# Optimization experiments

Hardware: AMD Instinct MI355X
Metric: run time of the kernel (lower is better)

Reference implementation:

```python
import jax, jax.numpy as jnp
import numpy as np

DIM = 1024
NUM_HEADS = 8
HEAD_DIM = 64
QK_DIM = NUM_HEADS * HEAD_DIM  # 512
B, S = 4, 1024


def setup_inputs() -> dict:
    key = jax.random.key(0)
    k1, k2, k3, k4, k5 = jax.random.split(key, 5)
    x = jax.random.normal(k1, (B, S, DIM), dtype=jnp.float32)
    mask = jax.random.randint(k2, (B, S), 0, 2).astype(bool)
    rotator = jax.random.normal(k3, (B, S, HEAD_DIM, HEAD_DIM), dtype=jnp.float32)
    # Linear weights stored as [in, out] for x @ W
    w_t = jax.random.normal(k4, (DIM, 2 * QK_DIM + DIM), dtype=jnp.float32) * (DIM ** -0.5)
    w_o = jax.random.normal(k5, (DIM, DIM), dtype=jnp.float32) * (DIM ** -0.5)
    return {"x": x, "mask": mask, "rotator": rotator, "w_t": w_t, "w_o": w_o}


def taylor_atn_fn(qs, ks, vs, mask):
    # 2nd-order Taylor approximation of softmax attention:
    # exp(s) ~= 1 + s + s^2/2, with invalid keys masked out.
    scale = HEAD_DIM ** -0.5
    s = jnp.einsum('bqhd,bkhd->bhqk', qs, ks) * scale  # [B,H,S,S]
    scores = 1.0 + s + 0.5 * s * s
    scores = scores * mask[:, None, None, :].astype(scores.dtype)  # mask keys
    denom = jnp.maximum(jnp.sum(scores, axis=-1), 1e-6)            # [B,H,Q]
    out = jnp.einsum('bhqk,bkhd->bqhd', scores, vs)
    out = out / jnp.transpose(denom, (0, 2, 1))[..., None]         # [B,Q,H,vd]
    return out.reshape(out.shape[0], out.shape[1], -1)


def reference(x, mask, rotator, w_t, w_o):
    t = x @ w_t                                   # [B,S,2*QK+DIM]
    Bx, Sx = t.shape[0], t.shape[1]
    qs = t[..., :QK_DIM].reshape(Bx, Sx, NUM_HEADS, HEAD_DIM)
    ks = t[..., QK_DIM:2 * QK_DIM].reshape(Bx, Sx, NUM_HEADS, HEAD_DIM)
    vs = t[..., 2 * QK_DIM:].reshape(Bx, Sx, NUM_HEADS, -1)
    m = mask[..., None, None]
    # masked per-position rotation: q -> R q, k -> R^T k
    qs = jnp.where(m, jnp.einsum('bsij,bshj->bshi', rotator, qs), qs)
    ks = jnp.where(m, jnp.einsum('bsij,bshi->bshj', rotator, ks), ks)
    out = taylor_atn_fn(qs, ks, vs, mask)
    return out @ w_o
```

## Files before the change

kernel.cpp:

```cpp
#include <hip/hip_runtime.h>
#include <cstdint>
#include <cstddef>

#define DIMX  1024
#define NH    8
#define HD    64
#define QKD   512
#define VDD   128
#define BATCH 4
#define SEQ   1024
#define NPOS  (BATCH*SEQ)
#define TW    (2*QKD + DIMX)
#define SCALE 0.125f

typedef __bf16 bf16x8 __attribute__((ext_vector_type(8)));
typedef float  f32x4  __attribute__((ext_vector_type(4)));
typedef float  f32x16 __attribute__((ext_vector_type(16)));

__device__ __forceinline__ ushort f2bf(float f) {
    unsigned b = __float_as_uint(f);
    return (ushort)((b + 0x7FFFu + ((b >> 16) & 1u)) >> 16);
}
__device__ __forceinline__ float bf2f(ushort u) {
    return __uint_as_float((unsigned)u << 16);
}

__device__ __forceinline__ unsigned cvtpk(float lo, float hi) {
    unsigned r;
    asm("v_cvt_pk_bf16_f32 %0, %1, %2" : "=v"(r) : "v"(lo), "v"(hi));
    return r;
}

__device__ __forceinline__ void plswap(unsigned &a, unsigned &b) {
    asm("v_permlane32_swap_b32 %0, %1" : "+v"(a), "+v"(b));
}

#define GLD16(src, dst) __builtin_amdgcn_global_load_lds(                      \
    (const __attribute__((address_space(1))) unsigned int*)(src),              \
    (__attribute__((address_space(3))) unsigned int*)(dst), 16, 0, 0)

#define SW(row, col) ((row)*64 + ((col) ^ (((row)&7)<<3)))

__device__ __forceinline__ int2 xcd_swz(int gx, int gy) {
    const int nwg = gx * gy;
    int id = blockIdx.y * gx + blockIdx.x;
    id = (id & 7) * (nwg >> 3) + (id >> 3);
    return make_int2(id % gx, id / gx);
}

__global__ __launch_bounds__(256)
void prep_all(const float* __restrict__ x, const float* __restrict__ w_t,
              const float* __restrict__ w_o, const int* __restrict__ mask,
              ushort* __restrict__ xbf, ushort* __restrict__ wtT,
              ushort* __restrict__ woT, int* __restrict__ cpos,
              int* __restrict__ nvalid)
{
    __shared__ float tile[32][33];
    const int bid = blockIdx.x;
    if (bid >= 5120) {
        const int b = bid - 5120;
        int* part = (int*)tile;
        const int t = threadIdx.x;
        int4 m = *(const int4*)(mask + b*SEQ + t*4);
        const int v0 = (m.x != 0), v1 = (m.y != 0);
        const int v2 = (m.z != 0), v3 = (m.w != 0);
        const int mine = v0 + v1 + v2 + v3;
        part[t] = mine;
        __syncthreads();
        for (int off = 1; off < 256; off <<= 1) {
            int y = (t >= off) ? part[t - off] : 0;
            __syncthreads();
            part[t] += y;
            __syncthreads();
        }
        const int ex = part[t] - mine;
        int4 o;
        o.x = v0 ? ex : -1;
        o.y = v1 ? ex + v0 : -1;
        o.z = v2 ? ex + v0 + v1 : -1;
        o.w = v3 ? ex + v0 + v1 + v2 : -1;
        *(int4*)(cpos + b*SEQ + t*4) = o;
        if (t == 255) nvalid[b] = part[255];
        return;
    }
    if (bid < 2048) {
        const size_t i = ((size_t)bid * 256 + threadIdx.x) * 8;
        float4 v0 = *(const float4*)(x + i);
        float4 v1 = *(const float4*)(x + i + 4);
        ushort o[8] = {f2bf(v0.x), f2bf(v0.y), f2bf(v0.z), f2bf(v0.w),
                       f2bf(v1.x), f2bf(v1.y), f2bf(v1.z), f2bf(v1.w)};
        *(uint4*)(xbf + i) = *(uint4*)o;
        return;
    }
    const float* W; ushort* WT; int K, N, bn, bk;
    if (bid < 4096) {
        W = w_t; WT = wtT; K = DIMX; N = TW;
        const int t = bid - 2048;
        bn = (t & 63) * 32; bk = (t >> 6) * 32;
    } else {
        W = w_o; WT = woT; K = DIMX; N = DIMX;
        const int t = bid - 4096;
        bn = (t & 31) * 32; bk = (t >> 5) * 32;
    }
    const int tx = threadIdx.x & 31;
    const int ty = threadIdx.x >> 5;
    #pragma unroll
    for (int i = ty; i < 32; i += 8)
        tile[i][tx] = W[(size_t)(bk + i) * N + bn + tx];
    __syncthreads();
    #pragma unroll
    for (int i = ty; i < 32; i += 8)
        WT[(size_t)(bn + i) * K + bk + tx] = f2bf(tile[tx][i]);
}

#define GEMM_PROLOGUE(Aptr, Bptr, Kdim)                                        \
    __shared__ __align__(16) ushort lA[2 * 128 * 64];                          \
    __shared__ __align__(16) ushort lB[2 * 128 * 64];                          \
    const int tid  = threadIdx.x;                                              \
    const int lane = tid & 63;                                                 \
    const int wave = tid >> 6;                                                 \
    const int wr   = wave >> 1;                                                \
    const int wc   = wave & 1;                                                 \
    const int rsub = lane >> 3;                        \
    const int scol = ((lane & 7) * 8) ^ ((rsub & 7) << 3);                     \
    const ushort* aP = (Aptr) + (size_t)(bm + wave*32 + rsub) * (Kdim) + scol; \
    const ushort* bP = (Bptr) + (size_t)(bn + wave*32 + rsub) * (Kdim) + scol; \
    ushort* lAw = lA + wave * 2048;                                            \
    ushort* lBw = lB + wave * 2048;                                            \
    const int fr = lane & 15;                                                  \
    const int l4 = lane >> 4;                                                  \
    f32x4 acc[4][4] = {};

#define GSTAGE(buf, k0, Kdim)                                                  \
    do {                                                                       \
        _Pragma("unroll")                                                      \
        for (int c = 0; c < 4; ++c) {                                          \
            GLD16(aP + (size_t)(c*8) * (Kdim) + (k0), lAw + (buf)*8192 + c*512);\
            GLD16(bP + (size_t)(c*8) * (Kdim) + (k0), lBw + (buf)*8192 + c*512);\
        }                                                                      \
    } while (0)

#define GEMM_KLOOP(Kdim)                                                       \
    GSTAGE(0, 0, Kdim);                                                        \
    for (int t = 0; t < (Kdim)/64; ++t) {                                      \
        const int cur = t & 1;                                                 \
        if (t < (Kdim)/64 - 1) {                                               \
            GSTAGE(cur ^ 1, (t + 1) * 64, Kdim);                               \
            asm volatile("s_waitcnt vmcnt(8)" ::: "memory");                   \
        } else {                                                               \
            asm volatile("s_waitcnt vmcnt(0)" ::: "memory");                   \
        }                                                                      \
        __builtin_amdgcn_s_barrier();               \
        _Pragma("unroll")                                                      \
        for (int ks = 0; ks < 2; ++ks) {                                       \
            bf16x8 af[4], bfr[4];                                              \
            _Pragma("unroll")                                                  \
            for (int m = 0; m < 4; ++m)                                        \
                af[m] = *(const bf16x8*)&lA[cur*8192 +                         \
                    SW(wr*64 + m*16 + fr, ks*32 + l4*8)];                      \
            _Pragma("unroll")                                                  \
            for (int n = 0; n < 4; ++n)                                        \
                bfr[n] = *(const bf16x8*)&lB[cur*8192 +                        \
                    SW(wc*64 + n*16 + fr, ks*32 + l4*8)];                      \
            _Pragma("unroll")                                                  \
            for (int m = 0; m < 4; ++m)                                        \
                _Pragma("unroll")                                              \
                for (int n = 0; n < 4; ++n)                                    \
                    acc[m][n] = __builtin_amdgcn_mfma_f32_16x16x32_bf16(       \
                        af[m], bfr[n], acc[m][n], 0, 0, 0);                    \
        }                                                                      \
        asm volatile("s_waitcnt lgkmcnt(0)" ::: "memory");                     \
        __builtin_amdgcn_s_barrier();             \
    }

__global__ __launch_bounds__(256, 2)
void gemm_qkv(const ushort* __restrict__ A, const ushort* __restrict__ BT,
              ushort* __restrict__ t1b, ushort* __restrict__ Vc,
              const int* __restrict__ cpos)
{
    const int2 bij = xcd_swz(TW/128, NPOS/128);
    const int bm = bij.y * 128;
    const int bn = bij.x * 128;
    GEMM_PROLOGUE(A, BT, DIMX)
    GEMM_KLOOP(DIMX)

    const int orow = l4 * 4;
    if (bn < 1024) {
        #pragma unroll
        for (int m = 0; m < 4; ++m)
            #pragma unroll
            for (int n = 0; n < 4; ++n) {
                ushort* dst = t1b + (size_t)(bm + wr * 64 + m * 16 + orow) * 1024
                                  + bn + wc * 64 + n * 16 + fr;
                #pragma unroll
                for (int q = 0; q < 4; ++q)
                    dst[(size_t)q * 1024] = f2bf(acc[m][n][q]);
            }
    } else {
        #pragma unroll
        for (int m = 0; m < 4; ++m)
            #pragma unroll
            for (int n = 0; n < 4; ++n) {
                const int row0 = bm + wr * 64 + m * 16 + orow;
                const int cv   = bn + wc * 64 + n * 16 + fr - 1024;
                const int hh = cv >> 7, vd = cv & 127;
                const int bb = row0 >> 10, ss = row0 & 1023;
                int4 cp = *(const int4*)(cpos + bb*SEQ + ss);
                ushort* vrow = Vc + ((size_t)(bb*NH + hh)*VDD + vd)*SEQ;
                if (cp.x >= 0) vrow[cp.x] = f2bf(acc[m][n][0]);
                if (cp.y >= 0) vrow[cp.y] = f2bf(acc[m][n][1]);
                if (cp.z >= 0) vrow[cp.z] = f2bf(acc[m][n][2]);
                if (cp.w >= 0) vrow[cp.w] = f2bf(acc[m][n][3]);
            }
    }
}

__global__ __launch_bounds__(256, 2)
void gemm_bf16_mfma(const ushort* __restrict__ A, const ushort* __restrict__ BT,
                    float* __restrict__ C)
{
    __shared__ __align__(16) ushort lA[2 * 64 * 64];
    __shared__ __align__(16) ushort lB[2 * 128 * 64];

    const int2 bij = xcd_swz(DIMX/128, NPOS/64);
    const int bm = bij.y * 64;
    const int bn = bij.x * 128;
    const int tid  = threadIdx.x;
    const int lane = tid & 63;
    const int wave = tid >> 6;
    const int wr   = wave >> 1;
    const int wc   = wave & 1;
    const int rsub = lane >> 3;
    const int scol = ((lane & 7) * 8) ^ ((rsub & 7) << 3);
    const ushort* aP = A  + (size_t)(bm + wave*16 + rsub) * DIMX + scol;
    const ushort* bP = BT + (size_t)(bn + wave*32 + rsub) * DIMX + scol;
    ushort* lAw = lA + wave * 1024;
    ushort* lBw = lB + wave * 2048;
    const int fr = lane & 15;
    const int l4 = lane >> 4;
    f32x4 acc[2][4] = {};

#define GSTAGE2(buf, k0) do {                                                  \
    _Pragma("unroll")                                                          \
    for (int c = 0; c < 2; ++c)                                                \
        GLD16(aP + (size_t)(c*8) * DIMX + (k0), lAw + (buf)*4096 + c*512);     \
    _Pragma("unroll")                                                          \
    for (int c = 0; c < 4; ++c)                                                \
        GLD16(bP + (size_t)(c*8) * DIMX + (k0), lBw + (buf)*8192 + c*512);     \
} while (0)

    GSTAGE2(0, 0);
    for (int t = 0; t < 16; ++t) {
        const int cur = t & 1;
        if (t < 15) {
            GSTAGE2(cur ^ 1, (t + 1) * 64);
            asm volatile("s_waitcnt vmcnt(6)" ::: "memory");
        } else {
            asm volatile("s_waitcnt vmcnt(0)" ::: "memory");
        }
        __builtin_amdgcn_s_barrier();
        #pragma unroll
        for (int ks = 0; ks < 2; ++ks) {
            bf16x8 af[2], bfr[4];
            #pragma unroll
            for (int m = 0; m < 2; ++m)
                af[m] = *(const bf16x8*)&lA[cur*4096 +
                    SW(wr*32 + m*16 + fr, ks*32 + l4*8)];
            #pragma unroll
            for (int n = 0; n < 4; ++n)
                bfr[n] = *(const bf16x8*)&lB[cur*8192 +
                    SW(wc*64 + n*16 + fr, ks*32 + l4*8)];
            #pragma unroll
            for (int m = 0; m < 2; ++m)
                #pragma unroll
                for (int n = 0; n < 4; ++n)
                    acc[m][n] = __builtin_amdgcn_mfma_f32_16x16x32_bf16(
                        af[m], bfr[n], acc[m][n], 0, 0, 0);
        }
        asm volatile("s_waitcnt lgkmcnt(0)" ::: "memory");
        __builtin_amdgcn_s_barrier();
    }
#undef GSTAGE2

    const int orow = l4 * 4;
    #pragma unroll
    for (int m = 0; m < 2; ++m)
        #pragma unroll
        for (int n = 0; n < 4; ++n) {
            float* dst = C + (size_t)(bm + wr*32 + m*16 + orow) * DIMX
                           + bn + wc*64 + n*16 + fr;
            #pragma unroll
            for (int q = 0; q < 4; ++q)
                dst[(size_t)q * DIMX] = acc[m][n][q];
        }
}

__global__ __launch_bounds__(256)
void rotate_pack_qk(const ushort* __restrict__ t1b, const int* __restrict__ mask,
                    const float* __restrict__ rot, ushort* __restrict__ Qb,
                    ushort* __restrict__ Kc, const int* __restrict__ cpos)
{
    const int p   = blockIdx.x;
    const int tid = threadIdx.x;
    const int b = p >> 10, s = p & 1023;
    const bool rotated = (mask[p] != 0);
    const int cp = cpos[p];

    if (!rotated) {
        if (tid < 128) {
            const int h  = tid >> 4;
            const int i4 = (tid & 15) * 4;
            ushort4 q4 = *(const ushort4*)(t1b + (size_t)p*1024 + tid*4);
            ushort o[4];
            o[0] = f2bf(bf2f(q4.x) * SCALE);
            o[1] = f2bf(bf2f(q4.y) * SCALE);
            o[2] = f2bf(bf2f(q4.z) * SCALE);
            o[3] = f2bf(bf2f(q4.w) * SCALE);
            *(ushort4*)&Qb[((size_t)(b*NH + h)*SEQ + s)*HD + i4] = *(ushort4*)o;
        }
        return;
    }

    __shared__ __align__(16) float Rsw [64*64];
    __shared__ __align__(16) float RTsw[64*64];

    {
        const int r  = tid >> 2;
        const int c0 = (tid & 3) * 16;
        const float* Rg = rot + (size_t)p * 4096 + (size_t)r * 64 + c0;
        #pragma unroll
        for (int u = 0; u < 4; ++u) {
            float4 v = *(const float4*)(Rg + 4*u);
            const int c4 = c0 + 4*u;
            *(float4*)&Rsw[r*64 + (c4 ^ ((r & 15) << 2))] = v;
            RTsw[(c4+0)*64 + (r ^ (((c4+0) & 15) << 2))] = v.x;
            RTsw[(c4+1)*64 + (r ^ (((c4+1) & 15) << 2))] = v.y;
            RTsw[(c4+2)*64 + (r ^ (((c4+2) & 15) << 2))] = v.z;
            RTsw[(c4+3)*64 + (r ^ (((c4+3) & 15) << 2))] = v.w;
        }
    }
    __syncthreads();

    const int i  = tid & 63;
    const int h0 = __builtin_amdgcn_readfirstlane(tid >> 6);
    const ushort* qg0 = t1b + (size_t)p*1024 + h0*64;
    const ushort* kg0 = t1b + (size_t)p*1024 + QKD + h0*64;
    const ushort* qg1 = qg0 + 4*64;
    const ushort* kg1 = kg0 + 4*64;

    float aq0 = 0.f, ak0 = 0.f, aq1 = 0.f, ak1 = 0.f;
    const int swk = (i & 15) << 2;
    #pragma unroll
    for (int jc = 0; jc < 16; ++jc) {
        const int j4 = jc * 4;
        const float4 Rv = *(const float4*)&Rsw [i*64 + (j4 ^ swk)];
        const float4 Tv = *(const float4*)&RTsw[i*64 + (j4 ^ swk)];
        const ushort4 qa = *(const ushort4*)(qg0 + j4);
        const ushort4 ka = *(const ushort4*)(kg0 + j4);
        const ushort4 qb = *(const ushort4*)(qg1 + j4);
        const ushort4 kb = *(const ushort4*)(kg1 + j4);
        aq0 = fmaf(Rv.x, bf2f(qa.x), aq0); aq0 = fmaf(Rv.y, bf2f(qa.y), aq0);
        aq0 = fmaf(Rv.z, bf2f(qa.z), aq0); aq0 = fmaf(Rv.w, bf2f(qa.w), aq0);
        ak0 = fmaf(Tv.x, bf2f(ka.x), ak0); ak0 = fmaf(Tv.y, bf2f(ka.y), ak0);
        ak0 = fmaf(Tv.z, bf2f(ka.z), ak0); ak0 = fmaf(Tv.w, bf2f(ka.w), ak0);
        aq1 = fmaf(Rv.x, bf2f(qb.x), aq1); aq1 = fmaf(Rv.y, bf2f(qb.y), aq1);
        aq1 = fmaf(Rv.z, bf2f(qb.z), aq1); aq1 = fmaf(Rv.w, bf2f(qb.w), aq1);
        ak1 = fmaf(Tv.x, bf2f(kb.x), ak1); ak1 = fmaf(Tv.y, bf2f(kb.y), ak1);
        ak1 = fmaf(Tv.z, bf2f(kb.z), ak1); ak1 = fmaf(Tv.w, bf2f(kb.w), ak1);
    }

    Qb[((size_t)(b*NH + h0    )*SEQ + s )*HD + i] = f2bf(aq0 * SCALE);
    Kc[((size_t)(b*NH + h0    )*SEQ + cp)*HD + i] = f2bf(ak0);
    Qb[((size_t)(b*NH + h0 + 4)*SEQ + s )*HD + i] = f2bf(aq1 * SCALE);
    Kc[((size_t)(b*NH + h0 + 4)*SEQ + cp)*HD + i] = f2bf(ak1);
}

__global__ __launch_bounds__(256, 2)
void taylor_attn_mfma(const ushort* __restrict__ Qb, const ushort* __restrict__ Kc,
                      const ushort* __restrict__ Vc, const int* __restrict__ nvalid,
                      ushort* __restrict__ attn)
{
    const int bh  = blockIdx.x;
    const int qt  = blockIdx.y;
    const int b   = bh >> 3, h = bh & 7;
    const int tid = threadIdx.x;
    const int lane = tid & 63;
    const int wave = tid >> 6;
    const int kh  = wave >> 1;
    const int qg  = wave & 1;
    const int l31 = lane & 31;
    const int g   = lane >> 5;

    __shared__ __align__(16) ushort smem[32768];
    __shared__ float dpart[64];
    __shared__ float dinv2[64];

    ushort* Ksp = smem + kh * 8192;
    ushort* Vsp = smem + 16384 + kh * 8192;
    float*  comb = (float*)smem;

    const int nv = nvalid[b];
    const int T  = (nv + 63) >> 6;
    const int Th = (T + 1) >> 1;

    const ushort* qrow = Qb + ((size_t)bh*SEQ + qt*64 + qg*32 + l31) * HD + g*8;
    bf16x8 qf[4];
    #pragma unroll
    for (int ds = 0; ds < 4; ++ds) qf[ds] = *(const bf16x8*)(qrow + ds*16);

    const int sub  = lane >> 3;
    const int scol = ((lane & 7) * 8) ^ (sub << 3);
    const ushort* Kbase = Kc + (size_t)bh*SEQ*HD;
    const ushort* Vbase = Vc + (size_t)bh*VDD*SEQ;

#define ISSUE_K(buf, ktn) do {                                                 \
    _Pragma("unroll")                                                          \
    for (int i_ = 0; i_ < 4; ++i_)                                             \
        GLD16(Kbase + ((size_t)(ktn)*64 + 8*(qg*4+i_) + sub)*HD + scol,        \
              Ksp + (buf)*4096 + (qg*4+i_)*512);                               \
} while (0)
#define ISSUE_V(ktn) do {                                                      \
    _Pragma("unroll")                                                          \
    for (int i_ = 0; i_ < 8; ++i_)                                             \
        GLD16(Vbase + (size_t)(8*(qg*8+i_) + sub)*SEQ + (ktn)*64 + scol,       \
              Vsp + (qg*8+i_)*512);                                            \
} while (0)

    f32x16 acc[4] = {};
    float dacc = 0.f;

    asm volatile("s_waitcnt vmcnt(0)" ::: "memory");
    ISSUE_K(0, kh*Th);

    for (int it = 0; it < Th; ++it) {
        const int kt = kh*Th + it;
        const int cb = it & 1;
        ISSUE_V(kt);
        if (it < Th - 1) {
            ISSUE_K(cb ^ 1, kt + 1);
            asm volatile("s_waitcnt vmcnt(12)" ::: "memory");
        } else {
            asm volatile("s_waitcnt vmcnt(8)"  ::: "memory");
        }
        __builtin_amdgcn_s_barrier();

        f32x16 sf0 = {}, sf1 = {};
        __builtin_amdgcn_s_setprio(1);
        #pragma unroll
        for (int ds = 0; ds < 4; ++ds) {
            const int dc = ds*16 + g*8;
            bf16x8 kf0 = *(const bf16x8*)&Ksp[cb*4096 + SW(l31, dc)];
            bf16x8 kf1 = *(const bf16x8*)&Ksp[cb*4096 + SW(32 + l31, dc)];
            sf0 = __builtin_amdgcn_mfma_f32_32x32x16_bf16(kf0, qf[ds], sf0, 0, 0, 0);
            sf1 = __builtin_amdgcn_mfma_f32_32x32x16_bf16(kf1, qf[ds], sf1, 0, 0, 0);
        }
        __builtin_amdgcn_s_setprio(0);

        const int kb0 = kt*64 + 4*g;
        unsigned w0[8], w1[8];
        float dadd = 0.f;
        #pragma unroll
        for (int rr = 0; rr < 4; ++rr) {
            const int ka = kb0 + 8*rr;
            const float ma0 = (ka + 0 < nv) ? 1.f : 0.f;
            const float ma1 = (ka + 1 < nv) ? 1.f : 0.f;
            const float ma2 = (ka + 2 < nv) ? 1.f : 0.f;
            const float ma3 = (ka + 3 < nv) ? 1.f : 0.f;
            const float mb0 = (ka + 32 < nv) ? 1.f : 0.f;
            const float mb1 = (ka + 33 < nv) ? 1.f : 0.f;
            const float mb2 = (ka + 34 < nv) ? 1.f : 0.f;
            const float mb3 = (ka + 35 < nv) ? 1.f : 0.f;
            float s0 = sf0[rr*4+0], s1 = sf0[rr*4+1];
            float s2 = sf0[rr*4+2], s3 = sf0[rr*4+3];
            float c0 = fmaf(fmaf(0.5f*s0, s0, s0), ma0, ma0);
            float c1 = fmaf(fmaf(0.5f*s1, s1, s1), ma1, ma1);
            float c2 = fmaf(fmaf(0.5f*s2, s2, s2), ma2, ma2);
            float c3 = fmaf(fmaf(0.5f*s3, s3, s3), ma3, ma3);
            float t0 = sf1[rr*4+0], t1 = sf1[rr*4+1];
            float t2 = sf1[rr*4+2], t3 = sf1[rr*4+3];
            float d0 = fmaf(fmaf(0.5f*t0, t0, t0), mb0, mb0);
            float d1 = fmaf(fmaf(0.5f*t1, t1, t1), mb1, mb1);
            float d2 = fmaf(fmaf(0.5f*t2, t2, t2), mb2, mb2);
            float d3 = fmaf(fmaf(0.5f*t3, t3, t3), mb3, mb3);
            dadd += ((c0+c1)+(c2+c3)) + ((d0+d1)+(d2+d3));
            w0[rr*2+0] = cvtpk(c0, c1);
            w0[rr*2+1] = cvtpk(c2, c3);
            w1[rr*2+0] = cvtpk(d0, d1);
            w1[rr*2+1] = cvtpk(d2, d3);
        }
        dacc += dadd;
        plswap(w0[0], w0[2]); plswap(w0[1], w0[3]);
        plswap(w0[4], w0[6]); plswap(w0[5], w0[7]);
        plswap(w1[0], w1[2]); plswap(w1[1], w1[3]);
        plswap(w1[4], w1[6]); plswap(w1[5], w1[7]);

        if (it < Th - 1) asm volatile("s_waitcnt vmcnt(4)" ::: "memory");
        else             asm volatile("s_waitcnt vmcnt(0)" ::: "memory");
        __builtin_amdgcn_s_barrier();

        __builtin_amdgcn_s_setprio(1);
        #pragma unroll
        for (int kq = 0; kq < 4; ++kq) {
            union { unsigned u[4]; bf16x8 v; } pu;
            if (kq == 0)      { pu.u[0]=w0[0]; pu.u[1]=w0[1]; pu.u[2]=w0[2]; pu.u[3]=w0[3]; }
            else if (kq == 1) { pu.u[0]=w0[4]; pu.u[1]=w0[5]; pu.u[2]=w0[6]; pu.u[3]=w0[7]; }
            else if (kq == 2) { pu.u[0]=w1[0]; pu.u[1]=w1[1]; pu.u[2]=w1[2]; pu.u[3]=w1[3]; }
            else              { pu.u[0]=w1[4]; pu.u[1]=w1[5]; pu.u[2]=w1[6]; pu.u[3]=w1[7]; }
            const int kcol = kq*16 + g*8;
            acc[0] = __builtin_amdgcn_mfma_f32_32x32x16_bf16(
                pu.v, *(const bf16x8*)&Vsp[SW(      l31, kcol)], acc[0], 0, 0, 0);
            acc[1] = __builtin_amdgcn_mfma_f32_32x32x16_bf16(
                pu.v, *(const bf16x8*)&Vsp[SW( 32 + l31, kcol)], acc[1], 0, 0, 0);
            acc[2] = __builtin_amdgcn_mfma_f32_32x32x16_bf16(
                pu.v, *(const bf16x8*)&Vsp[SW( 64 + l31, kcol)], acc[2], 0, 0, 0);
            acc[3] = __builtin_amdgcn_mfma_f32_32x32x16_bf16(
                pu.v, *(const bf16x8*)&Vsp[SW( 96 + l31, kcol)], acc[3], 0, 0, 0);
        }
        __builtin_amdgcn_s_setprio(0);
        __builtin_amdgcn_s_barrier();
    }
#undef ISSUE_K
#undef ISSUE_V

    const float dhalf = dacc + __shfl_xor(dacc, 32);

    if (kh == 1) {
        float* cbp = comb + qg * 4096;
        #pragma unroll
        for (int vb = 0; vb < 4; ++vb)
            #pragma unroll
            for (int rr = 0; rr < 4; ++rr) {
                float4 v = make_float4(acc[vb][rr*4+0], acc[vb][rr*4+1],
                                       acc[vb][rr*4+2], acc[vb][rr*4+3]);
                *(float4*)&cbp[(vb*32 + l31)*32 + 4*g + 8*rr] = v;
            }
        if (lane < 32) dpart[qg*32 + l31] = dhalf;
    }
    __syncthreads();
    if (kh == 0) {
        float* cbp = comb + qg * 4096;
        const float dtot = dhalf + dpart[qg*32 + l31];
        if (lane < 32) dinv2[qg*32 + l31] = 1.f / fmaxf(dtot, 1e-6f);
        #pragma unroll
        for (int vb = 0; vb < 4; ++vb)
            #pragma unroll
            for (int rr = 0; rr < 4; ++rr) {
                float4 v = *(const float4*)&cbp[(vb*32 + l31)*32 + 4*g + 8*rr];
                acc[vb][rr*4+0] += v.x; acc[vb][rr*4+1] += v.y;
                acc[vb][rr*4+2] += v.z; acc[vb][rr*4+3] += v.w;
            }
        float inv[16];
        #pragma unroll
        for (int rr = 0; rr < 4; ++rr) {
            float4 iv = *(const float4*)&dinv2[qg*32 + 8*rr + 4*g];
            inv[rr*4+0] = iv.x; inv[rr*4+1] = iv.y;
            inv[rr*4+2] = iv.z; inv[rr*4+3] = iv.w;
        }
        ushort* obase = attn + ((size_t)(b*SEQ + qt*64 + qg*32)) * DIMX
                      + h*VDD + l31;
        #pragma unroll
        for (int vb = 0; vb < 4; ++vb)
            #pragma unroll
            for (int rr = 0; rr < 4; ++rr)
                #pragma unroll
                for (int j = 0; j < 4; ++j) {
                    const int q = 4*g + 8*rr + j;
                    obase[(size_t)q*DIMX + vb*32] = f2bf(acc[vb][rr*4+j] * inv[rr*4+j]);
                }
    }
}

extern "C" void kernel_launch(void* const* d_in, const int* in_sizes, int n_in,
                              void* d_out, int out_size, void* d_ws, size_t ws_size,
                              hipStream_t stream)
{
    const float* x    = (const float*)d_in[0];
    const int*   mask = (const int*)d_in[1];
    const float* rot  = (const float*)d_in[2];
    const float* w_t  = (const float*)d_in[3];
    const float* w_o  = (const float*)d_in[4];
    float* out = (float*)d_out;

    ushort* t1b    = (ushort*)d_ws;
    ushort* xbf    = t1b + (size_t)NPOS * 1024;
    ushort* attnbf = xbf;
    ushort* wtT    = xbf + (size_t)NPOS * DIMX;
    ushort* woT    = wtT + (size_t)TW * DIMX;
    ushort* Qb     = woT + (size_t)DIMX * DIMX;
    ushort* Kc     = Qb  + (size_t)BATCH * NH * SEQ * HD;
    ushort* Vc     = Kc  + (size_t)BATCH * NH * SEQ * HD;
    int*    cpos   = (int*)(Vc + (size_t)BATCH * NH * VDD * SEQ);
    int*    nvalid = cpos + NPOS;

    prep_all<<<5124, 256, 0, stream>>>(x, w_t, w_o, mask, xbf, wtT, woT,
                                       cpos, nvalid);

    gemm_qkv<<<dim3(TW/128, NPOS/128), 256, 0, stream>>>(xbf, wtT, t1b, Vc, cpos);
    rotate_pack_qk<<<NPOS, 256, 0, stream>>>(t1b, mask, rot, Qb, Kc, cpos);
    taylor_attn_mfma<<<dim3(BATCH*NH, SEQ/64), 256, 0, stream>>>(Qb, Kc, Vc,
                                                                 nvalid, attnbf);
    gemm_bf16_mfma<<<dim3(DIMX/128, NPOS/64), 256, 0, stream>>>(attnbf, woT, out);
}
```

Baseline: 90.05 us.

## Write V transposed densely in GEMM epilogue, compact valid keys in separate kernel

The QKV GEMM epilogue used to scatter V values one element at a time into compacted positions, looking up cpos for every row. It now writes dense transposed V with 8-byte vector stores, and a new compact_v kernel gathers only the valid sequence positions through an inverse index (spos) built in prep_all. This replaces scattered 2-byte global stores with coalesced writes, at the cost of an extra kernel launch and an extra read and write pass over V.

After: 98.01 us. 1.09x slower.

```diff
diff --git a/kernel.cpp b/kernel.cpp
--- a/kernel.cpp
+++ b/kernel.cpp
@@ -53,7 +53,7 @@
               const float* __restrict__ w_o, const int* __restrict__ mask,
               ushort* __restrict__ xbf, ushort* __restrict__ wtT,
               ushort* __restrict__ woT, int* __restrict__ cpos,
-              int* __restrict__ nvalid)
+              int* __restrict__ spos, int* __restrict__ nvalid)
 {
     __shared__ float tile[32][33];
     const int bid = blockIdx.x;
@@ -80,6 +80,10 @@
         o.z = v2 ? ex + v0 + v1 : -1;
         o.w = v3 ? ex + v0 + v1 + v2 : -1;
         *(int4*)(cpos + b*SEQ + t*4) = o;
+        if (v0) spos[b*SEQ + o.x] = t*4 + 0;
+        if (v1) spos[b*SEQ + o.y] = t*4 + 1;
+        if (v2) spos[b*SEQ + o.z] = t*4 + 2;
+        if (v3) spos[b*SEQ + o.w] = t*4 + 3;
         if (t == 255) nvalid[b] = part[255];
         return;
     }
@@ -175,8 +179,7 @@
 
 __global__ __launch_bounds__(256, 2)
 void gemm_qkv(const ushort* __restrict__ A, const ushort* __restrict__ BT,
-              ushort* __restrict__ t1b, ushort* __restrict__ Vc,
-              const int* __restrict__ cpos)
+              ushort* __restrict__ t1b, ushort* __restrict__ Vt)
 {
     const int2 bij = xcd_swz(TW/128, NPOS/128);
     const int bm = bij.y * 128;
@@ -205,13 +208,38 @@
                 const int cv   = bn + wc * 64 + n * 16 + fr - 1024;
                 const int hh = cv >> 7, vd = cv & 127;
                 const int bb = row0 >> 10, ss = row0 & 1023;
-                int4 cp = *(const int4*)(cpos + bb*SEQ + ss);
-                ushort* vrow = Vc + ((size_t)(bb*NH + hh)*VDD + vd)*SEQ;
-                if (cp.x >= 0) vrow[cp.x] = f2bf(acc[m][n][0]);
-                if (cp.y >= 0) vrow[cp.y] = f2bf(acc[m][n][1]);
-                if (cp.z >= 0) vrow[cp.z] = f2bf(acc[m][n][2]);
-                if (cp.w >= 0) vrow[cp.w] = f2bf(acc[m][n][3]);
+                ushort o4[4];
+                #pragma unroll
+                for (int q = 0; q < 4; ++q) o4[q] = f2bf(acc[m][n][q]);
+                *(ushort4*)&Vt[((size_t)(bb*NH + hh)*VDD + vd)*SEQ + ss] =
+                    *(ushort4*)o4;
             }
+    }
+}
+
+__global__ __launch_bounds__(256)
+void compact_v(const ushort* __restrict__ Vt, const int* __restrict__ spos,
+               const int* __restrict__ nvalid, ushort* __restrict__ Vc)
+{
+    const int bh = blockIdx.x;
+    const int vg = blockIdx.y;
+    const int b  = bh >> 3;
+    const int tid = threadIdx.x;
+    const int nv = nvalid[b];
+
+    __shared__ int sps[SEQ];
+    for (int i = tid; i < nv; i += 256) sps[i] = spos[b*SEQ + i];
+    __syncthreads();
+
+    const ushort* src = Vt + (size_t)bh*VDD*SEQ;
+    ushort* dst = Vc + (size_t)bh*VDD*SEQ;
+    #pragma unroll
+    for (int v = 0; v < 16; ++v) {
+        const int vd = vg*16 + v;
+        const ushort* srow = src + (size_t)vd*SEQ;
+        ushort* drow = dst + (size_t)vd*SEQ;
+        for (int ci = tid; ci < nv; ci += 256)
+            drow[ci] = srow[sps[ci]];
     }
 }
 
@@ -588,14 +616,17 @@
     ushort* woT    = wtT + (size_t)TW * DIMX;
     ushort* Qb     = woT + (size_t)DIMX * DIMX;
     ushort* Kc     = Qb  + (size_t)BATCH * NH * SEQ * HD;
-    ushort* Vc     = Kc  + (size_t)BATCH * NH * SEQ * HD;
+    ushort* Vt     = Kc  + (size_t)BATCH * NH * SEQ * HD;
+    ushort* Vc     = Vt  + (size_t)BATCH * NH * VDD * SEQ;
     int*    cpos   = (int*)(Vc + (size_t)BATCH * NH * VDD * SEQ);
-    int*    nvalid = cpos + NPOS;
+    int*    spos   = cpos + NPOS;
+    int*    nvalid = spos + NPOS;
 
     prep_all<<<5124, 256, 0, stream>>>(x, w_t, w_o, mask, xbf, wtT, woT,
-                                       cpos, nvalid);
-
-    gemm_qkv<<<dim3(TW/128, NPOS/128), 256, 0, stream>>>(xbf, wtT, t1b, Vc, cpos);
+                                       cpos, spos, nvalid);
+
+    gemm_qkv<<<dim3(TW/128, NPOS/128), 256, 0, stream>>>(xbf, wtT, t1b, Vt);
+    compact_v<<<dim3(BATCH*NH, 8), 256, 0, stream>>>(Vt, spos, nvalid, Vc);
     rotate_pack_qk<<<NPOS, 256, 0, stream>>>(t1b, mask, rot, Qb, Kc, cpos);
     taylor_attn_mfma<<<dim3(BATCH*NH, SEQ/64), 256, 0, stream>>>(Qb, Kc, Vc,
                                                                  nvalid, attnbf);
```
